# Performance work log

Measured on AMD Instinct MI355X. Metric: run time of the kernel, lower is better.

Reference implementation:

```python
import jax, jax.numpy as jnp
import numpy as np
from jax.scipy.linalg import solve_triangular

H = 4          # num_heads
CHUNK = 64     # delta-rule chunk size (math-equivalent to any chunking)
NORM_EPS = 1e-5


def setup_inputs() -> dict:
    key = jax.random.key(0)
    ks = jax.random.split(key, 9)
    B, L, D = 4, 4096, 1024
    dk, dv = 512, 1024
    s = 0.02  # ~ xavier_uniform gain 2**-2.5 scale
    return {
        "hidden_states": jax.random.normal(ks[0], (B, L, D), jnp.float32),
        "conv_w": jax.random.normal(ks[1], (D, 4), jnp.float32) * 0.2,
        "Wq": jax.random.normal(ks[2], (D, dk), jnp.float32) * s,
        "Wk": jax.random.normal(ks[3], (D, dk), jnp.float32) * s,
        "Wv": jax.random.normal(ks[4], (D, dv), jnp.float32) * s,
        "Wb": jax.random.normal(ks[5], (D, H), jnp.float32) * s,
        "Wg": jax.random.normal(ks[6], (D, dv), jnp.float32) * s,
        "norm_w": jnp.ones((dv // H,), jnp.float32),
        "Wo": jax.random.normal(ks[7], (dv, D), jnp.float32) * s,
    }


def _l2norm(x):
    return x / jnp.clip(jnp.linalg.norm(x, axis=-1, keepdims=True), 1e-12)


def _deltanet_forward(hidden_states, conv_w, Wq, Wk, Wv, Wb, Wg, norm_w, Wo):
    B, L, D = hidden_states.shape
    Kc = conv_w.shape[1]
    dqh = Wq.shape[1] // H   # head qk dim (128)
    dvh = Wv.shape[1] // H   # head v dim (256)

    # shared causal depthwise short conv + silu (ShortConvolution)
    xp = jnp.pad(hidden_states, ((0, 0), (Kc - 1, 0), (0, 0)))
    h = sum(conv_w[:, i] * xp[:, i:i + L, :] for i in range(Kc))
    h = jax.nn.silu(h)

    q = (h @ Wq).reshape(B, L, H, dqh).transpose(0, 2, 1, 3)  # b h l d
    k = (h @ Wk).reshape(B, L, H, dqh).transpose(0, 2, 1, 3)
    v = (h @ Wv).reshape(B, L, H, dvh).transpose(0, 2, 1, 3)
    q = _l2norm(q)
    k = _l2norm(k)
    beta = jax.nn.sigmoid(h @ Wb).transpose(0, 2, 1)          # b h l

    qm = q.reshape(B * H, L, dqh)
    km = k.reshape(B * H, L, dqh)
    vm = v.reshape(B * H, L, dvh)
    bm = beta.reshape(B * H, L)

    Nc = L // CHUNK
    eye = jnp.eye(CHUNK, dtype=q.dtype)

    def per_head(qh, kh, vh, bh):
        qs = qh.reshape(Nc, CHUNK, dqh)
        ks_ = kh.reshape(Nc, CHUNK, dqh)
        vs = vh.reshape(Nc, CHUNK, dvh)
        bs = bh.reshape(Nc, CHUNK)

        def step(S, xs):
            qc, kc, vc, bc = xs
            kb = kc * bc[:, None]
            # (I + strict_tril(kb k^T)) U = beta*(V - K S)  -> exact delta rule
            A = jnp.tril(kb @ kc.T, -1)
            U = solve_triangular(eye + A, vc * bc[:, None] - kb @ S, lower=True)
            o = qc @ S + jnp.tril(qc @ kc.T) @ U
            return S + kc.T @ U, o

        S0 = jnp.zeros((dqh, dvh), qh.dtype)
        _, o = jax.lax.scan(step, S0, (qs, ks_, vs, bs))
        return o.reshape(L, dvh)

    o = jax.vmap(per_head)(qm, km, vm, bm)                    # (B*H, L, dvh)
    o = o.reshape(B, H, L, dvh).transpose(0, 2, 1, 3)         # b l h d

    # FusedRMSNormSwishGate: rmsnorm(o) * weight * silu(g)
    g = (h @ Wg).reshape(B, L, H, dvh)
    rms = o * jax.lax.rsqrt(jnp.mean(o * o, axis=-1, keepdims=True) + NORM_EPS)
    out = rms * norm_w * (g * jax.nn.sigmoid(g))
    return out.reshape(B, L, H * dvh) @ Wo


def reference(hidden_states, conv_w, Wq, Wk, Wv, Wb, Wg, norm_w, Wo):
    return _deltanet_forward(hidden_states, conv_w, Wq, Wk, Wv, Wb, Wg, norm_w, Wo)
```

## Files before the change

### kernel.cpp

```cpp
#include <hip/hip_runtime.h>
#include <math.h>

constexpr int Lseq = 4096, Dm = 1024, H = 4, DK = 512, DV = 1024;
constexpr int DQH = 128, DVH = 256, CH = 64, ROWS = 4 * 4096;

typedef unsigned short u16;
struct alignas(16) us8 { u16 u[8]; };
typedef __attribute__((ext_vector_type(8))) short bf16x8;
typedef __attribute__((ext_vector_type(4))) float f32x4;

__device__ __forceinline__ float sig_(float x) { return 1.f / (1.f + expf(-x)); }
__device__ __forceinline__ float b2f(u16 u) {
  union { float f; unsigned v; } x; x.v = (unsigned)u << 16; return x.f;
}
__device__ __forceinline__ u16 f2b(float f) {
  union { float f; unsigned v; } x; x.f = f;
  unsigned r = x.v + 0x7fffu + ((x.v >> 16) & 1u);
  return (u16)(r >> 16);
}
__device__ __forceinline__ void gld16(const u16* g, u16* l) {
  __builtin_amdgcn_global_load_lds(
      (const __attribute__((address_space(1))) void*)g,
      (__attribute__((address_space(3))) void*)l, 16, 0, 0);
}

__global__ void ws_sentinel_kernel(float* out, float v) { out[0] = v; }

__global__ __launch_bounds__(256) void cvt_t_kernel(
    const float* __restrict__ in, u16* __restrict__ out, int N, int K) {
  __shared__ u16 T[32][66];
  const int k0 = blockIdx.y * 32, n0 = blockIdx.x * 64;
  const int t = threadIdx.x;
#pragma unroll
  for (int i = 0; i < 8; ++i) {
    int idx = t + i * 256;
    int kk = idx >> 6, nn = idx & 63;
    T[kk][nn] = f2b(in[(size_t)(k0 + kk) * N + n0 + nn]);
  }
  __syncthreads();
#pragma unroll
  for (int i = 0; i < 8; ++i) {
    int idx = t + i * 256;
    int kk = idx & 31, nn = idx >> 5;
    out[(size_t)(n0 + nn) * K + k0 + kk] = T[kk][nn];
  }
}

__global__ __launch_bounds__(256) void conv_silu_kernel(
    const float* __restrict__ x, const float* __restrict__ w, u16* __restrict__ h) {
  int idx = blockIdx.x * 256 + threadIdx.x;
  int d8 = (idx & 127) << 3;
  int row = idx >> 7;
  int l = row & (Lseq - 1), b = row >> 12;
  const float* xb = x + ((size_t)b << 22);
  float4 wv[8];
#pragma unroll
  for (int j = 0; j < 2; ++j) {
    wv[j * 4 + 0] = *(const float4*)&w[d8 * 4 + j * 16 + 0];
    wv[j * 4 + 1] = *(const float4*)&w[d8 * 4 + j * 16 + 4];
    wv[j * 4 + 2] = *(const float4*)&w[d8 * 4 + j * 16 + 8];
    wv[j * 4 + 3] = *(const float4*)&w[d8 * 4 + j * 16 + 12];
  }
  float acc[8] = {0, 0, 0, 0, 0, 0, 0, 0};
#pragma unroll
  for (int i = 0; i < 4; ++i) {
    int li = l - 3 + i;
    if (li >= 0) {
      float4 x0 = *(const float4*)&xb[((size_t)li << 10) + d8];
      float4 x1 = *(const float4*)&xb[((size_t)li << 10) + d8 + 4];
      acc[0] = fmaf(((const float*)&wv[0])[i], x0.x, acc[0]);
      acc[1] = fmaf(((const float*)&wv[1])[i], x0.y, acc[1]);
      acc[2] = fmaf(((const float*)&wv[2])[i], x0.z, acc[2]);
      acc[3] = fmaf(((const float*)&wv[3])[i], x0.w, acc[3]);
      acc[4] = fmaf(((const float*)&wv[4])[i], x1.x, acc[4]);
      acc[5] = fmaf(((const float*)&wv[5])[i], x1.y, acc[5]);
      acc[6] = fmaf(((const float*)&wv[6])[i], x1.z, acc[6]);
      acc[7] = fmaf(((const float*)&wv[7])[i], x1.w, acc[7]);
    }
  }
  us8 o;
#pragma unroll
  for (int j = 0; j < 8; ++j) o.u[j] = f2b(acc[j] * sig_(acc[j]));
  *(us8*)&h[(size_t)row * Dm + d8] = o;
}

template <int MODE>
__global__ __launch_bounds__(256) void gemm_mfma_kernel(
    const u16* __restrict__ A, const u16* __restrict__ BT, void* __restrict__ Cv,
    int M, int N, int K) {
  __shared__ u16 As[128 * 64];
  __shared__ u16 Bs[128 * 64];
  const int tid = threadIdx.x;
  const int wid = tid >> 6, lane = tid & 63;
  const int wr = wid >> 1, wc = wid & 1;
  const int fr = lane & 15, fk = lane >> 4;
  const int nbx = N >> 7;
  const int bid = blockIdx.x, nwg = gridDim.x;
  const int swz = (bid & 7) * (nwg >> 3) + (bid >> 3);
  const int row0 = (swz / nbx) * 128, col0 = (swz % nbx) * 128;

  int sr[4], sk[4];
#pragma unroll
  for (int i = 0; i < 4; ++i) {
    int s = i * 4 + wid;
    int r = s * 8 + (lane >> 3);
    sr[i] = r;
    sk[i] = ((lane & 7) ^ (r & 7)) << 3;
  }

  f32x4 acc[4][4];
#pragma unroll
  for (int i = 0; i < 4; ++i)
#pragma unroll
    for (int j = 0; j < 4; ++j) acc[i][j] = {0.f, 0.f, 0.f, 0.f};

  for (int k0 = 0; k0 < K; k0 += 64) {
#pragma unroll
    for (int i = 0; i < 4; ++i) {
      const int s = i * 4 + wid;
      gld16(&A[(size_t)(row0 + sr[i]) * K + k0 + sk[i]], &As[s * 512]);
      gld16(&BT[(size_t)(col0 + sr[i]) * K + k0 + sk[i]], &Bs[s * 512]);
    }
    __syncthreads();
#pragma unroll
    for (int kt = 0; kt < 2; ++kt) {
      bf16x8 af[4], bf[4];
#pragma unroll
      for (int mi = 0; mi < 4; ++mi) {
        int row = wr * 64 + mi * 16 + fr;
        af[mi] = *(const bf16x8*)&As[row * 64 + (((kt * 4 + fk) ^ (fr & 7)) << 3)];
      }
#pragma unroll
      for (int ni = 0; ni < 4; ++ni) {
        int row = wc * 64 + ni * 16 + fr;
        bf[ni] = *(const bf16x8*)&Bs[row * 64 + (((kt * 4 + fk) ^ (fr & 7)) << 3)];
      }
#pragma unroll
      for (int mi = 0; mi < 4; ++mi)
#pragma unroll
        for (int ni = 0; ni < 4; ++ni)
          acc[mi][ni] = __builtin_amdgcn_mfma_f32_16x16x32_bf16(
              af[mi], bf[ni], acc[mi][ni], 0, 0, 0);
    }
    __syncthreads();
  }

  if (MODE == 2) {
    __shared__ float ssh[2][128];
#pragma unroll
    for (int mi = 0; mi < 4; ++mi)
#pragma unroll
      for (int r = 0; r < 4; ++r) {
        float p = 0.f;
#pragma unroll
        for (int ni = 0; ni < 4; ++ni) p += acc[mi][ni][r] * acc[mi][ni][r];
        p += __shfl_xor(p, 1); p += __shfl_xor(p, 2);
        p += __shfl_xor(p, 4); p += __shfl_xor(p, 8);
        if (fr == 0) ssh[wc][wr * 64 + mi * 16 + fk * 4 + r] = p;
      }
    __syncthreads();
#pragma unroll
    for (int mi = 0; mi < 4; ++mi)
#pragma unroll
      for (int r = 0; r < 4; ++r) {
        int ridx = wr * 64 + mi * 16 + fk * 4 + r;
        float sc = 1.f / fmaxf(sqrtf(ssh[0][ridx] + ssh[1][ridx]), 1e-12f);
#pragma unroll
        for (int ni = 0; ni < 4; ++ni) acc[mi][ni][r] *= sc;
      }
  }

#pragma unroll
  for (int mi = 0; mi < 4; ++mi)
#pragma unroll
    for (int ni = 0; ni < 4; ++ni) {
      int col = col0 + wc * 64 + ni * 16 + fr;
#pragma unroll
      for (int r = 0; r < 4; ++r) {
        int row = row0 + wr * 64 + mi * 16 + fk * 4 + r;
        if (MODE == 1) ((float*)Cv)[(size_t)row * N + col] = acc[mi][ni][r];
        else           ((u16*)Cv)[(size_t)row * N + col] = f2b(acc[mi][ni][r]);
      }
    }
}

__global__ __launch_bounds__(256) void beta_kernel(
    const u16* __restrict__ h, const float* __restrict__ Wb, float* __restrict__ beta) {
  int row = blockIdx.x * 4 + (threadIdx.x >> 6), lane = threadIdx.x & 63;
  const u16* hrow = h + (size_t)row * Dm;
  float a0 = 0, a1 = 0, a2 = 0, a3 = 0;
  for (int k0 = 0; k0 < Dm; k0 += 64) {
    float hv = b2f(hrow[k0 + lane]);
    float4 wv = *(const float4*)&Wb[(size_t)(k0 + lane) * 4];
    a0 = fmaf(hv, wv.x, a0); a1 = fmaf(hv, wv.y, a1);
    a2 = fmaf(hv, wv.z, a2); a3 = fmaf(hv, wv.w, a3);
  }
#pragma unroll
  for (int off = 32; off; off >>= 1) {
    a0 += __shfl_down(a0, off); a1 += __shfl_down(a1, off);
    a2 += __shfl_down(a2, off); a3 += __shfl_down(a3, off);
  }
  if (lane == 0) {
    int b = row >> 12, l = row & (Lseq - 1);
    beta[((size_t)(b * H + 0)) * Lseq + l] = sig_(a0);
    beta[((size_t)(b * H + 1)) * Lseq + l] = sig_(a1);
    beta[((size_t)(b * H + 2)) * Lseq + l] = sig_(a2);
    beta[((size_t)(b * H + 3)) * Lseq + l] = sig_(a3);
  }
}

__global__ __launch_bounds__(256) void delta_prep_kernel(
    const u16* __restrict__ q, const u16* __restrict__ k,
    u16* v, const float* __restrict__ beta,
    u16* __restrict__ Wout, u16* __restrict__ QKout) {
  __shared__ alignas(16) char lds0[18432];
  __shared__ alignas(16) char lds1[18432];
  __shared__ float Bc[64];
  float (*Am)[68] = (float(*)[68])lds0;
  float (*R)[68]  = (float(*)[68])lds1;
  u16 (*Th)[72]  = (u16(*)[72])lds0;
  u16 (*Tl)[72]  = (u16(*)[72])(lds0 + 9216);
  u16 (*XTh)[72] = (u16(*)[72])lds1;
  u16 (*XTl)[72] = (u16(*)[72])(lds1 + 9216);

  const int tid = threadIdx.x;
  const int wid = tid >> 6, lane = tid & 63;
  const int fr = lane & 15, fq = lane >> 4;
  const int bh = blockIdx.x >> 6, ch = blockIdx.x & 63;
  const int b = bh >> 2, hh = bh & 3;
  const int c0 = ch * CH;
  const u16* qbase = q + (size_t)b * Lseq * DK + hh * DQH;
  const u16* kbase = k + (size_t)b * Lseq * DK + hh * DQH;
  u16*       vbase = v + (size_t)b * Lseq * DV + hh * DVH;
  const float* bbase = beta + (size_t)bh * Lseq;
  u16* Wrow  = Wout  + ((size_t)bh * Lseq + c0) * DQH;
  u16* QKrow = QKout + ((size_t)bh * Lseq + c0) * CH;

  if (tid < 64) Bc[tid] = bbase[c0 + tid];
  for (int idx = tid; idx < 64 * 64; idx += 256) {
    int r = idx >> 6, c = idx & 63;
    R[r][c] = (r == c) ? 1.f : 0.f;
  }
  __syncthreads();

  {
    const int m0 = wid * 16;
    f32x4 accG[4], accQ[4];
#pragma unroll
    for (int ni = 0; ni < 4; ++ni) {
      accG[ni] = {0.f, 0.f, 0.f, 0.f};
      accQ[ni] = {0.f, 0.f, 0.f, 0.f};
    }
#pragma unroll
    for (int kt = 0; kt < 4; ++kt) {
      bf16x8 afk = *(const bf16x8*)&kbase[(size_t)(c0 + m0 + fr) * DK + kt * 32 + fq * 8];
      bf16x8 afq = *(const bf16x8*)&qbase[(size_t)(c0 + m0 + fr) * DK + kt * 32 + fq * 8];
#pragma unroll
      for (int ni = 0; ni < 4; ++ni) {
        bf16x8 bfk = *(const bf16x8*)&kbase[(size_t)(c0 + ni * 16 + fr) * DK + kt * 32 + fq * 8];
        accG[ni] = __builtin_amdgcn_mfma_f32_16x16x32_bf16(afk, bfk, accG[ni], 0, 0, 0);
        accQ[ni] = __builtin_amdgcn_mfma_f32_16x16x32_bf16(afq, bfk, accQ[ni], 0, 0, 0);
      }
    }
#pragma unroll
    for (int ni = 0; ni < 4; ++ni)
#pragma unroll
      for (int i = 0; i < 4; ++i) {
        int row = m0 + fq * 4 + i, col = ni * 16 + fr;
        float br = Bc[row];
        Am[row][col] = (col < row) ? br * accG[ni][i] : 0.f;
        QKrow[(size_t)row * CH + col] = f2b((col <= row) ? accQ[ni][i] : 0.f);
      }
  }
  __syncthreads();

  for (int rb = 0; rb < 4; ++rb) {
    if (rb > 0) {
      const int c = tid & 63, g = tid >> 6;
      const int R0 = rb * 16, row = R0 + g * 4;
      float s0 = 0, s1 = 0, s2 = 0, s3 = 0;
      for (int m = 0; m < R0; ++m) {
        float uv = R[m][c];
        s0 = fmaf(Am[row + 0][m], uv, s0);
        s1 = fmaf(Am[row + 1][m], uv, s1);
        s2 = fmaf(Am[row + 2][m], uv, s2);
        s3 = fmaf(Am[row + 3][m], uv, s3);
      }
      R[row + 0][c] -= s0; R[row + 1][c] -= s1;
      R[row + 2][c] -= s2; R[row + 3][c] -= s3;
    }
    __syncthreads();
    if (tid < 64) {
      const int c = tid;
      for (int i = 1; i < 16; ++i) {
        const int row = rb * 16 + i;
        float s = R[row][c];
        for (int m = 0; m < i; ++m)
          s = fmaf(-Am[row][rb * 16 + m], R[rb * 16 + m][c], s);
        R[row][c] = s;
      }
    }
    __syncthreads();
  }

  for (int idx = tid; idx < 64 * 64; idx += 256) {
    int r = idx >> 6, c = idx & 63;
    float tv = R[r][c];
    u16 hh2 = f2b(tv);
    Th[r][c] = hh2;
    Tl[r][c] = f2b(tv - b2f(hh2));
  }
  __syncthreads();

  for (int p = 0; p < 6; ++p) {
    const int off = (p < 2) ? p * 64 : (p - 2) * 64;
    for (int idx = tid; idx < 64 * 64; idx += 256) {
      int d = idx & 63, m = idx >> 6;
      float xv;
      if (p < 2) xv = Bc[m] * b2f(kbase[(size_t)(c0 + m) * DK + off + d]);
      else       xv = Bc[m] * b2f(vbase[(size_t)(c0 + m) * DV + off + d]);
      u16 hh2 = f2b(xv);
      XTh[d][m] = hh2;
      XTl[d][m] = f2b(xv - b2f(hh2));
    }
    __syncthreads();
    f32x4 acc[4];
#pragma unroll
    for (int tn = 0; tn < 4; ++tn) acc[tn] = {0.f, 0.f, 0.f, 0.f};
#pragma unroll
    for (int kt = 0; kt < 2; ++kt) {
      bf16x8 ah = *(const bf16x8*)&Th[wid * 16 + fr][kt * 32 + fq * 8];
      bf16x8 al = *(const bf16x8*)&Tl[wid * 16 + fr][kt * 32 + fq * 8];
#pragma unroll
      for (int tn = 0; tn < 4; ++tn) {
        bf16x8 xh = *(const bf16x8*)&XTh[tn * 16 + fr][kt * 32 + fq * 8];
        bf16x8 xl = *(const bf16x8*)&XTl[tn * 16 + fr][kt * 32 + fq * 8];
        acc[tn] = __builtin_amdgcn_mfma_f32_16x16x32_bf16(ah, xh, acc[tn], 0, 0, 0);
        acc[tn] = __builtin_amdgcn_mfma_f32_16x16x32_bf16(ah, xl, acc[tn], 0, 0, 0);
        acc[tn] = __builtin_amdgcn_mfma_f32_16x16x32_bf16(al, xh, acc[tn], 0, 0, 0);
      }
    }
#pragma unroll
    for (int tn = 0; tn < 4; ++tn)
#pragma unroll
      for (int i = 0; i < 4; ++i) {
        int row = wid * 16 + fq * 4 + i, col = tn * 16 + fr;
        if (p < 2) Wrow[(size_t)row * DQH + off + col] = f2b(-acc[tn][i]);
        else       vbase[(size_t)(c0 + row) * DV + off + col] = f2b(acc[tn][i]);
      }
    __syncthreads();
  }
}

__global__ __launch_bounds__(512) void delta_scan_kernel(
    const u16* __restrict__ q, const u16* __restrict__ k,
    const u16* __restrict__ Wb, const u16* __restrict__ QKb, u16* uo) {
  __shared__ alignas(16) u16 Kt[128][72];
  __shared__ alignas(16) u16 Sbt_hi[16][136];
  __shared__ alignas(16) u16 Sbt_lo[16][136];
  __shared__ alignas(16) u16 Ubt[16][72];
  const int tid = threadIdx.x;
  const int wid = tid >> 6, lane = tid & 63;
  const int fr = lane & 15, fq = lane >> 4;
  const int m0w = 16 * (wid & 3);
  const int bh = blockIdx.x & 15, vblk = blockIdx.x >> 4;
  const int b = bh >> 2, hh = bh & 3;
  const u16* qbase = q + (size_t)b * Lseq * DK + hh * DQH;
  const u16* kbase = k + (size_t)b * Lseq * DK + hh * DQH;
  const u16* Wbase = Wb + (size_t)bh * Lseq * DQH;
  const u16* QKbase = QKb + (size_t)bh * Lseq * CH;
  u16* uobase = uo + (size_t)b * Lseq * DV + hh * DVH + vblk * 16;

  for (int i = tid; i < 16 * 136; i += 512) {
    (&Sbt_hi[0][0])[i] = 0; (&Sbt_lo[0][0])[i] = 0;
  }
  f32x4 Sfrag = {0.f, 0.f, 0.f, 0.f};

  const int kr0 = tid & 63, kd0 = (tid >> 6) << 3;
  const int kr1 = (tid + 512) & 63, kd1 = ((tid + 512) >> 6) << 3;

  us8 kpre0 = *(const us8*)&kbase[(size_t)kr0 * DK + kd0];
  us8 kpre1 = *(const us8*)&kbase[(size_t)kr1 * DK + kd1];
  bf16x8 fpre[4];
  bf16x8 qkpre0 = {}, qkpre1 = {};
  ushort4 u0pre = {};
  if (wid < 4) {
    const u16* wp = Wbase + (size_t)(m0w + fr) * DQH + fq * 8;
#pragma unroll
    for (int kt = 0; kt < 4; ++kt) fpre[kt] = *(const bf16x8*)&wp[kt * 32];
    const u16* up = uobase + (size_t)(m0w + fq * 4) * DV + fr;
    u0pre.x = up[0]; u0pre.y = up[(size_t)DV];
    u0pre.z = up[(size_t)2 * DV]; u0pre.w = up[(size_t)3 * DV];
  } else {
    const u16* qp = qbase + (size_t)(m0w + fr) * DK + fq * 8;
#pragma unroll
    for (int kt = 0; kt < 4; ++kt) fpre[kt] = *(const bf16x8*)&qp[kt * 32];
    const u16* qkp = QKbase + (size_t)(m0w + fr) * CH + fq * 8;
    qkpre0 = *(const bf16x8*)&qkp[0];
    qkpre1 = *(const bf16x8*)&qkp[32];
  }
  __syncthreads();

  for (int c0 = 0; c0 < Lseq; c0 += CH) {
#pragma unroll
    for (int j = 0; j < 8; ++j) Kt[kd0 + j][kr0] = kpre0.u[j];
#pragma unroll
    for (int j = 0; j < 8; ++j) Kt[kd1 + j][kr1] = kpre1.u[j];

    bf16x8 fcur[4];
#pragma unroll
    for (int kt = 0; kt < 4; ++kt) fcur[kt] = fpre[kt];
    bf16x8 qkc0 = qkpre0, qkc1 = qkpre1;
    ushort4 u0c = u0pre;

    if (c0 + CH < Lseq) {
      const int cn = c0 + CH;
      kpre0 = *(const us8*)&kbase[(size_t)(cn + kr0) * DK + kd0];
      kpre1 = *(const us8*)&kbase[(size_t)(cn + kr1) * DK + kd1];
      if (wid < 4) {
        const u16* wp = Wbase + (size_t)(cn + m0w + fr) * DQH + fq * 8;
#pragma unroll
        for (int kt = 0; kt < 4; ++kt) fpre[kt] = *(const bf16x8*)&wp[kt * 32];
        const u16* up = uobase + (size_t)(cn + m0w + fq * 4) * DV + fr;
        u0pre.x = up[0]; u0pre.y = up[(size_t)DV];
        u0pre.z = up[(size_t)2 * DV]; u0pre.w = up[(size_t)3 * DV];
      } else {
        const u16* qp = qbase + (size_t)(cn + m0w + fr) * DK + fq * 8;
#pragma unroll
        for (int kt = 0; kt < 4; ++kt) fpre[kt] = *(const bf16x8*)&qp[kt * 32];
        const u16* qkp = QKbase + (size_t)(cn + m0w + fr) * CH + fq * 8;
        qkpre0 = *(const bf16x8*)&qkp[0];
        qkpre1 = *(const bf16x8*)&qkp[32];
      }
    }

    f32x4 acc, accB;
    if (wid < 4) {
      acc[0] = b2f(u0c.x); acc[1] = b2f(u0c.y);
      acc[2] = b2f(u0c.z); acc[3] = b2f(u0c.w);
      accB = (f32x4){0.f, 0.f, 0.f, 0.f};
      __builtin_amdgcn_s_setprio(1);
#pragma unroll
      for (int kt = 0; kt < 2; ++kt) {
        bf16x8 sh = *(const bf16x8*)&Sbt_hi[fr][kt * 32 + fq * 8];
        bf16x8 sl = *(const bf16x8*)&Sbt_lo[fr][kt * 32 + fq * 8];
        acc = __builtin_amdgcn_mfma_f32_16x16x32_bf16(fcur[kt], sh, acc, 0, 0, 0);
        acc = __builtin_amdgcn_mfma_f32_16x16x32_bf16(fcur[kt], sl, acc, 0, 0, 0);
      }
#pragma unroll
      for (int kt = 2; kt < 4; ++kt) {
        bf16x8 sh = *(const bf16x8*)&Sbt_hi[fr][kt * 32 + fq * 8];
        bf16x8 sl = *(const bf16x8*)&Sbt_lo[fr][kt * 32 + fq * 8];
        accB = __builtin_amdgcn_mfma_f32_16x16x32_bf16(fcur[kt], sh, accB, 0, 0, 0);
        accB = __builtin_amdgcn_mfma_f32_16x16x32_bf16(fcur[kt], sl, accB, 0, 0, 0);
      }
      __builtin_amdgcn_s_setprio(0);
      ushort4 ub = {f2b(acc[0] + accB[0]), f2b(acc[1] + accB[1]),
                    f2b(acc[2] + accB[2]), f2b(acc[3] + accB[3])};
      *(ushort4*)&Ubt[fr][m0w + fq * 4] = ub;
    } else {
      acc = (f32x4){0.f, 0.f, 0.f, 0.f};
      accB = (f32x4){0.f, 0.f, 0.f, 0.f};
#pragma unroll
      for (int kt = 0; kt < 2; ++kt) {
        bf16x8 sh = *(const bf16x8*)&Sbt_hi[fr][kt * 32 + fq * 8];
        acc = __builtin_amdgcn_mfma_f32_16x16x32_bf16(fcur[kt], sh, acc, 0, 0, 0);
      }
#pragma unroll
      for (int kt = 2; kt < 4; ++kt) {
        bf16x8 sh = *(const bf16x8*)&Sbt_hi[fr][kt * 32 + fq * 8];
        accB = __builtin_amdgcn_mfma_f32_16x16x32_bf16(fcur[kt], sh, accB, 0, 0, 0);
      }
    }
    __syncthreads();

    if (wid >= 4) {
      bf16x8 uf0 = *(const bf16x8*)&Ubt[fr][fq * 8];
      bf16x8 uf1 = *(const bf16x8*)&Ubt[fr][32 + fq * 8];
      acc  = __builtin_amdgcn_mfma_f32_16x16x32_bf16(qkc0, uf0, acc, 0, 0, 0);
      accB = __builtin_amdgcn_mfma_f32_16x16x32_bf16(qkc1, uf1, accB, 0, 0, 0);
      u16* op = uobase + (size_t)(c0 + m0w + fq * 4) * DV + fr;
      op[0] = f2b(acc[0] + accB[0]);
      op[(size_t)DV] = f2b(acc[1] + accB[1]);
      op[(size_t)2 * DV] = f2b(acc[2] + accB[2]);
      op[(size_t)3 * DV] = f2b(acc[3] + accB[3]);
    }
    __builtin_amdgcn_s_setprio(1);
#pragma unroll
    for (int kt = 0; kt < 2; ++kt) {
      bf16x8 kf = *(const bf16x8*)&Kt[16 * wid + fr][kt * 32 + fq * 8];
      bf16x8 uf = *(const bf16x8*)&Ubt[fr][kt * 32 + fq * 8];
      Sfrag = __builtin_amdgcn_mfma_f32_16x16x32_bf16(kf, uf, Sfrag, 0, 0, 0);
    }
    __builtin_amdgcn_s_setprio(0);
    ushort4 shv, slv;
#pragma unroll
    for (int i = 0; i < 4; ++i) {
      float s = Sfrag[i];
      u16 hpart = f2b(s);
      ((u16*)&shv)[i] = hpart;
      ((u16*)&slv)[i] = f2b(s - b2f(hpart));
    }
    *(ushort4*)&Sbt_hi[fr][16 * wid + fq * 4] = shv;
    *(ushort4*)&Sbt_lo[fr][16 * wid + fq * 4] = slv;
    __syncthreads();
  }
}

__global__ __launch_bounds__(256) void gate_kernel(
    const u16* og, const u16* __restrict__ g,
    const float* __restrict__ nw, u16* out) {
  int idx = blockIdx.x * 4 + (threadIdx.x >> 6), lane = threadIdx.x & 63;
  size_t base = (size_t)(idx >> 2) * DV + (size_t)(idx & 3) * DVH + (size_t)lane * 4;
  ushort4 o4 = *(const ushort4*)&og[base];
  float ox = b2f(o4.x), oy = b2f(o4.y), oz = b2f(o4.z), ow = b2f(o4.w);
  float ss = ox * ox + oy * oy + oz * oz + ow * ow;
#pragma unroll
  for (int off = 32; off; off >>= 1) ss += __shfl_xor(ss, off);
  float r = 1.f / sqrtf(ss * (1.f / DVH) + 1e-5f);
  ushort4 g4 = *(const ushort4*)&g[base];
  float gx = b2f(g4.x), gy = b2f(g4.y), gz = b2f(g4.z), gw = b2f(g4.w);
  float4 wv = *(const float4*)&nw[lane * 4];
  ushort4 res;
  res.x = f2b(ox * r * wv.x * (gx * sig_(gx)));
  res.y = f2b(oy * r * wv.y * (gy * sig_(gy)));
  res.z = f2b(oz * r * wv.z * (gz * sig_(gz)));
  res.w = f2b(ow * r * wv.w * (gw * sig_(gw)));
  *(ushort4*)&out[base] = res;
}

extern "C" void kernel_launch(void* const* d_in, const int* in_sizes, int n_in,
                              void* d_out, int out_size, void* d_ws, size_t ws_size,
                              hipStream_t stream) {
  (void)in_sizes; (void)n_in; (void)out_size;
  const float* x  = (const float*)d_in[0];
  const float* cw = (const float*)d_in[1];
  const float* Wq = (const float*)d_in[2];
  const float* Wk = (const float*)d_in[3];
  const float* Wv = (const float*)d_in[4];
  const float* Wb = (const float*)d_in[5];
  const float* Wg = (const float*)d_in[6];
  const float* nw = (const float*)d_in[7];
  const float* Wo = (const float*)d_in[8];
  float* out = (float*)d_out;

  u16* hb = (u16*)d_ws;
  u16* qb = hb + (size_t)ROWS * Dm;
  u16* kb = qb + (size_t)ROWS * DK;
  u16* vb = kb + (size_t)ROWS * DK;
  float* bbuf = (float*)(vb + (size_t)ROWS * DV);
  u16* Wbuf  = (u16*)(bbuf + (size_t)ROWS * H);
  u16* QKbuf = Wbuf + (size_t)16 * Lseq * DQH;
  u16* wq16 = QKbuf + (size_t)16 * Lseq * CH;
  u16* wk16 = wq16 + (size_t)Dm * DK;
  u16* wv16 = wk16 + (size_t)Dm * DK;
  u16* wg16 = wv16 + (size_t)Dm * DV;
  u16* wo16 = wg16 + (size_t)Dm * DV;
  u16* gb = qb;

  const size_t need = (size_t)ROWS * (Dm + DK + DK + DV) * 2 + (size_t)ROWS * H * 4
                    + (size_t)16 * Lseq * (DQH + CH) * 2
                    + ((size_t)Dm * (DK * 2 + DV * 3)) * 2;
  if (ws_size < need) {
    ws_sentinel_kernel<<<1, 1, 0, stream>>>(out, (float)ws_size);
    return;
  }

  cvt_t_kernel<<<dim3(DK / 64, Dm / 32), 256, 0, stream>>>(Wq, wq16, DK, Dm);
  cvt_t_kernel<<<dim3(DK / 64, Dm / 32), 256, 0, stream>>>(Wk, wk16, DK, Dm);
  cvt_t_kernel<<<dim3(DV / 64, Dm / 32), 256, 0, stream>>>(Wv, wv16, DV, Dm);
  cvt_t_kernel<<<dim3(DV / 64, Dm / 32), 256, 0, stream>>>(Wg, wg16, DV, Dm);
  cvt_t_kernel<<<dim3(Dm / 64, DV / 32), 256, 0, stream>>>(Wo, wo16, Dm, DV);

  conv_silu_kernel<<<ROWS * Dm / 8 / 256, 256, 0, stream>>>(x, cw, hb);

  gemm_mfma_kernel<2><<<(DK / 128) * (ROWS / 128), 256, 0, stream>>>(hb, wq16, qb, ROWS, DK, Dm);
  gemm_mfma_kernel<2><<<(DK / 128) * (ROWS / 128), 256, 0, stream>>>(hb, wk16, kb, ROWS, DK, Dm);
  gemm_mfma_kernel<0><<<(DV / 128) * (ROWS / 128), 256, 0, stream>>>(hb, wv16, vb, ROWS, DV, Dm);
  beta_kernel<<<ROWS / 4, 256, 0, stream>>>(hb, Wb, bbuf);

  delta_prep_kernel<<<1024, 256, 0, stream>>>(qb, kb, vb, bbuf, Wbuf, QKbuf);
  delta_scan_kernel<<<256, 512, 0, stream>>>(qb, kb, Wbuf, QKbuf, vb);

  gemm_mfma_kernel<0><<<(DV / 128) * (ROWS / 128), 256, 0, stream>>>(hb, wg16, gb, ROWS, DV, Dm);
  gate_kernel<<<ROWS * H / 4, 256, 0, stream>>>(vb, gb, nw, vb);

  gemm_mfma_kernel<1><<<(Dm / 128) * (ROWS / 128), 256, 0, stream>>>(vb, wo16, out, ROWS, Dm, DV);
}
```

Measured before the change: 517.7 us.

## Co-schedule delta scan with gate projection GEMM in one launch

The delta scan uses only 256 blocks. The new kernel appends 1024 GEMM blocks that compute h@Wg into a separate workspace buffer, so the Wg projection fills idle CUs while the latency-bound scan runs. The five weight-conversion launches are also merged into one kernel. The fused path needs extra workspace and falls back to the old sequence if it is missing. Shared-memory use per block grows for the scan blocks, which may lower their occupancy.

```diff
diff --git a/kernel.cpp b/kernel.cpp
--- a/kernel.cpp
+++ b/kernel.cpp
@@ -26,10 +26,21 @@
 
 __global__ void ws_sentinel_kernel(float* out, float v) { out[0] = v; }
 
-__global__ __launch_bounds__(256) void cvt_t_kernel(
-    const float* __restrict__ in, u16* __restrict__ out, int N, int K) {
+__global__ __launch_bounds__(256) void cvt_all_kernel(
+    const float* __restrict__ Wq, const float* __restrict__ Wk,
+    const float* __restrict__ Wv, const float* __restrict__ Wg,
+    const float* __restrict__ Wo,
+    u16* wq16, u16* wk16, u16* wv16, u16* wg16, u16* wo16) {
   __shared__ u16 T[32][66];
-  const int k0 = blockIdx.y * 32, n0 = blockIdx.x * 64;
+  int bid = blockIdx.x;
+  const float* in; u16* out; int N, K, b0;
+  if (bid < 256)       { in = Wq; out = wq16; N = DK; K = Dm; b0 = bid; }
+  else if (bid < 512)  { in = Wk; out = wk16; N = DK; K = Dm; b0 = bid - 256; }
+  else if (bid < 1024) { in = Wv; out = wv16; N = DV; K = Dm; b0 = bid - 512; }
+  else if (bid < 1536) { in = Wg; out = wg16; N = DV; K = Dm; b0 = bid - 1024; }
+  else                 { in = Wo; out = wo16; N = Dm; K = DV; b0 = bid - 1536; }
+  const int nbx = N / 64;
+  const int k0 = (b0 / nbx) * 32, n0 = (b0 % nbx) * 64;
   const int t = threadIdx.x;
 #pragma unroll
   for (int i = 0; i < 8; ++i) {
@@ -352,18 +363,15 @@
   }
 }
 
-__global__ __launch_bounds__(512) void delta_scan_kernel(
-    const u16* __restrict__ q, const u16* __restrict__ k,
-    const u16* __restrict__ Wb, const u16* __restrict__ QKb, u16* uo) {
-  __shared__ alignas(16) u16 Kt[128][72];
-  __shared__ alignas(16) u16 Sbt_hi[16][136];
-  __shared__ alignas(16) u16 Sbt_lo[16][136];
-  __shared__ alignas(16) u16 Ubt[16][72];
+__device__ __forceinline__ void scan_body(
+    int sbid, const u16* __restrict__ q, const u16* __restrict__ k,
+    const u16* __restrict__ Wb, const u16* __restrict__ QKb, u16* uo,
+    u16 (*Kt)[72], u16 (*Sbt_hi)[136], u16 (*Sbt_lo)[136], u16 (*Ubt)[72]) {
   const int tid = threadIdx.x;
   const int wid = tid >> 6, lane = tid & 63;
   const int fr = lane & 15, fq = lane >> 4;
   const int m0w = 16 * (wid & 3);
-  const int bh = blockIdx.x & 15, vblk = blockIdx.x >> 4;
+  const int bh = sbid & 15, vblk = sbid >> 4;
   const int b = bh >> 2, hh = bh & 3;
   const u16* qbase = q + (size_t)b * Lseq * DK + hh * DQH;
   const u16* kbase = k + (size_t)b * Lseq * DK + hh * DQH;
@@ -505,6 +513,98 @@
     *(ushort4*)&Sbt_lo[fr][16 * wid + fq * 4] = slv;
     __syncthreads();
   }
+}
+
+__global__ __launch_bounds__(512) void delta_scan_kernel(
+    const u16* __restrict__ q, const u16* __restrict__ k,
+    const u16* __restrict__ Wb, const u16* __restrict__ QKb, u16* uo) {
+  __shared__ alignas(16) u16 Kt[128][72];
+  __shared__ alignas(16) u16 Sbt_hi[16][136];
+  __shared__ alignas(16) u16 Sbt_lo[16][136];
+  __shared__ alignas(16) u16 Ubt[16][72];
+  scan_body(blockIdx.x, q, k, Wb, QKb, uo, Kt, Sbt_hi, Sbt_lo, Ubt);
+}
+
+__global__ __launch_bounds__(512) void scan_wg_kernel(
+    const u16* __restrict__ q, const u16* __restrict__ k,
+    const u16* __restrict__ Wb, const u16* __restrict__ QKb, u16* uo,
+    const u16* __restrict__ A, const u16* __restrict__ BT, u16* __restrict__ C) {
+  __shared__ alignas(16) u16 Kt[128][72];
+  __shared__ alignas(16) u16 Sbt_hi[16][136];
+  __shared__ alignas(16) u16 Sbt_lo[16][136];
+  __shared__ alignas(16) u16 Ubt[16][72];
+  __shared__ u16 As[128 * 64];
+  __shared__ u16 Bs[128 * 64];
+
+  if (blockIdx.x < 256) {
+    scan_body(blockIdx.x, q, k, Wb, QKb, uo, Kt, Sbt_hi, Sbt_lo, Ubt);
+    return;
+  }
+  const int tid = threadIdx.x;
+  const int wid = tid >> 6, lane = tid & 63;
+  const int wr = wid >> 2, wc = wid & 3;
+  const int fr = lane & 15, fk = lane >> 4;
+  const int nbx = DV >> 7;
+  const int gbid = blockIdx.x - 256, nwg = 1024;
+  const int swz = (gbid & 7) * (nwg >> 3) + (gbid >> 3);
+  const int row0 = (swz / nbx) * 128, col0 = (swz % nbx) * 128;
+
+  int sr[2], sk[2];
+#pragma unroll
+  for (int i = 0; i < 2; ++i) {
+    int s = i * 8 + wid;
+    int r = s * 8 + (lane >> 3);
+    sr[i] = r;
+    sk[i] = ((lane & 7) ^ (r & 7)) << 3;
+  }
+
+  f32x4 acc[4][2];
+#pragma unroll
+  for (int i = 0; i < 4; ++i)
+#pragma unroll
+    for (int j = 0; j < 2; ++j) acc[i][j] = {0.f, 0.f, 0.f, 0.f};
+
+  for (int k0 = 0; k0 < Dm; k0 += 64) {
+#pragma unroll
+    for (int i = 0; i < 2; ++i) {
+      const int s = i * 8 + wid;
+      gld16(&A[(size_t)(row0 + sr[i]) * Dm + k0 + sk[i]], &As[s * 512]);
+      gld16(&BT[(size_t)(col0 + sr[i]) * Dm + k0 + sk[i]], &Bs[s * 512]);
+    }
+    __syncthreads();
+#pragma unroll
+    for (int kt = 0; kt < 2; ++kt) {
+      bf16x8 af[4], bf[2];
+#pragma unroll
+      for (int mi = 0; mi < 4; ++mi) {
+        int row = wr * 64 + mi * 16 + fr;
+        af[mi] = *(const bf16x8*)&As[row * 64 + (((kt * 4 + fk) ^ (fr & 7)) << 3)];
+      }
+#pragma unroll
+      for (int ni = 0; ni < 2; ++ni) {
+        int row = wc * 32 + ni * 16 + fr;
+        bf[ni] = *(const bf16x8*)&Bs[row * 64 + (((kt * 4 + fk) ^ (fr & 7)) << 3)];
+      }
+#pragma unroll
+      for (int mi = 0; mi < 4; ++mi)
+#pragma unroll
+        for (int ni = 0; ni < 2; ++ni)
+          acc[mi][ni] = __builtin_amdgcn_mfma_f32_16x16x32_bf16(
+              af[mi], bf[ni], acc[mi][ni], 0, 0, 0);
+    }
+    __syncthreads();
+  }
+#pragma unroll
+  for (int mi = 0; mi < 4; ++mi)
+#pragma unroll
+    for (int ni = 0; ni < 2; ++ni) {
+      int col = col0 + wc * 32 + ni * 16 + fr;
+#pragma unroll
+      for (int r = 0; r < 4; ++r) {
+        int row = row0 + wr * 64 + mi * 16 + fk * 4 + r;
+        C[(size_t)row * DV + col] = f2b(acc[mi][ni][r]);
+      }
+    }
 }
 
 __global__ __launch_bounds__(256) void gate_kernel(
@@ -556,22 +656,21 @@
   u16* wv16 = wk16 + (size_t)Dm * DK;
   u16* wg16 = wv16 + (size_t)Dm * DV;
   u16* wo16 = wg16 + (size_t)Dm * DV;
-  u16* gb = qb;
+  u16* gb2  = wo16 + (size_t)DV * Dm;
+  u16* gb   = qb;
 
   const size_t need = (size_t)ROWS * (Dm + DK + DK + DV) * 2 + (size_t)ROWS * H * 4
                     + (size_t)16 * Lseq * (DQH + CH) * 2
                     + ((size_t)Dm * (DK * 2 + DV * 3)) * 2;
+  const size_t need2 = need + (size_t)ROWS * DV * 2;
   if (ws_size < need) {
     ws_sentinel_kernel<<<1, 1, 0, stream>>>(out, (float)ws_size);
     return;
   }
-
-  cvt_t_kernel<<<dim3(DK / 64, Dm / 32), 256, 0, stream>>>(Wq, wq16, DK, Dm);
-  cvt_t_kernel<<<dim3(DK / 64, Dm / 32), 256, 0, stream>>>(Wk, wk16, DK, Dm);
-  cvt_t_kernel<<<dim3(DV / 64, Dm / 32), 256, 0, stream>>>(Wv, wv16, DV, Dm);
-  cvt_t_kernel<<<dim3(DV / 64, Dm / 32), 256, 0, stream>>>(Wg, wg16, DV, Dm);
-  cvt_t_kernel<<<dim3(Dm / 64, DV / 32), 256, 0, stream>>>(Wo, wo16, Dm, DV);
-
+  const bool fused = (ws_size >= need2);
+
+  cvt_all_kernel<<<2048, 256, 0, stream>>>(Wq, Wk, Wv, Wg, Wo,
+                                           wq16, wk16, wv16, wg16, wo16);
   conv_silu_kernel<<<ROWS * Dm / 8 / 256, 256, 0, stream>>>(x, cw, hb);
 
   gemm_mfma_kernel<2><<<(DK / 128) * (ROWS / 128), 256, 0, stream>>>(hb, wq16, qb, ROWS, DK, Dm);
@@ -580,10 +679,15 @@
   beta_kernel<<<ROWS / 4, 256, 0, stream>>>(hb, Wb, bbuf);
 
   delta_prep_kernel<<<1024, 256, 0, stream>>>(qb, kb, vb, bbuf, Wbuf, QKbuf);
-  delta_scan_kernel<<<256, 512, 0, stream>>>(qb, kb, Wbuf, QKbuf, vb);
-
-  gemm_mfma_kernel<0><<<(DV / 128) * (ROWS / 128), 256, 0, stream>>>(hb, wg16, gb, ROWS, DV, Dm);
-  gate_kernel<<<ROWS * H / 4, 256, 0, stream>>>(vb, gb, nw, vb);
+
+  if (fused) {
+    scan_wg_kernel<<<1280, 512, 0, stream>>>(qb, kb, Wbuf, QKbuf, vb, hb, wg16, gb2);
+    gate_kernel<<<ROWS * H / 4, 256, 0, stream>>>(vb, gb2, nw, vb);
+  } else {
+    delta_scan_kernel<<<256, 512, 0, stream>>>(qb, kb, Wbuf, QKbuf, vb);
+    gemm_mfma_kernel<0><<<(DV / 128) * (ROWS / 128), 256, 0, stream>>>(hb, wg16, gb, ROWS, DV, Dm);
+    gate_kernel<<<ROWS * H / 4, 256, 0, stream>>>(vb, gb, nw, vb);
+  }
 
   gemm_mfma_kernel<1><<<(Dm / 128) * (ROWS / 128), 256, 0, stream>>>(vb, wo16, out, ROWS, Dm, DV);
 }
```

Result: faster. 480.0 us (-7.3%).
